# Kernel tuning notes

Hardware: AMD Instinct MI355X
Metric: run time of the kernel (lower is better)

## Reference

```python
import jax, jax.numpy as jnp
import numpy as np


def setup_inputs() -> dict:
    key = jax.random.key(0)
    k1, k2 = jax.random.split(key)
    B, La, Lb, D = 32, 512, 512, 768
    a_bar = jax.random.normal(k1, (B, La, D), dtype=jnp.float32)
    b_bar = jax.random.normal(k2, (B, Lb, D), dtype=jnp.float32)
    return {"a_bar": a_bar, "b_bar": b_bar}


def reference(a_bar, b_bar):
    # e: [B, La, Lb] cross-attention scores
    e = jnp.einsum('bad,bcd->bac', a_bar, b_bar)
    # attend over b positions (softmax dim=2) -> aligned representation of a
    a_tilde = jnp.einsum('bac,bcd->bad', jax.nn.softmax(e, axis=2), b_bar)
    # attend over a positions (softmax dim=1), transpose, bmm with a_bar
    b_tilde = jnp.einsum('bac,bad->bcd', jax.nn.softmax(e, axis=1), a_bar)
    m_a = jnp.concatenate([a_bar, a_tilde, a_bar - a_tilde, a_bar * a_tilde], axis=-1)
    m_b = jnp.concatenate([b_bar, b_tilde, b_bar - b_tilde, b_bar * b_tilde], axis=-1)
    return (m_a, m_b)
```

## Files before the change

kernel.cpp:

```cpp
#include <hip/hip_runtime.h>
#include <hip/hip_bf16.h>
#include <math.h>

#define NB 32
#define LA 512
#define LB 512
#define DD 768

typedef __bf16 bf16x4 __attribute__((ext_vector_type(4)));
typedef __bf16 bf16x8 __attribute__((ext_vector_type(8)));
typedef float f32x4 __attribute__((ext_vector_type(4)));

#define LSTR 40

__global__ __launch_bounds__(256) void gemm_e_mfma(
    const float* __restrict__ A, const float* __restrict__ Bm,
    float* __restrict__ E) {
  __shared__ __bf16 Ah[128][LSTR], Al[128][LSTR];
  __shared__ __bf16 Bh[128][LSTR], Bl[128][LSTR];

  const int b = blockIdx.z;
  const int i0 = blockIdx.x * 128, j0 = blockIdx.y * 128;
  const float* Ab = A + (size_t)b * LA * DD;
  const float* Bb = Bm + (size_t)b * LB * DD;
  float* Eb = E + (size_t)b * LA * LB;

  const int t = threadIdx.x;
  const int lane = t & 63, wave = t >> 6;
  const int wm = (wave >> 1) * 64, wn = (wave & 1) * 64;
  const int quad = lane >> 4, l16 = lane & 15;
  const int sr = t >> 3, sc = t & 7;

  f32x4 acc[4][4] = {};

  for (int k0 = 0; k0 < DD; k0 += 32) {
    float4 av[4], bv[4];
#pragma unroll
    for (int p = 0; p < 4; ++p) {
      av[p] = *(const float4*)(Ab + (size_t)(i0 + sr + p * 32) * DD + k0 + sc * 4);
      bv[p] = *(const float4*)(Bb + (size_t)(j0 + sr + p * 32) * DD + k0 + sc * 4);
    }
    __syncthreads();
#pragma unroll
    for (int p = 0; p < 4; ++p) {
      const int m = sr + p * 32;
      float va[4] = {av[p].x, av[p].y, av[p].z, av[p].w};
      float vb[4] = {bv[p].x, bv[p].y, bv[p].z, bv[p].w};
      bf16x4 ha, la, hb, lb;
#pragma unroll
      for (int q = 0; q < 4; ++q) {
        __bf16 h = (__bf16)va[q];
        ha[q] = h; la[q] = (__bf16)(va[q] - (float)h);
        h = (__bf16)vb[q];
        hb[q] = h; lb[q] = (__bf16)(vb[q] - (float)h);
      }
      *(bf16x4*)&Ah[m][sc * 4] = ha; *(bf16x4*)&Al[m][sc * 4] = la;
      *(bf16x4*)&Bh[m][sc * 4] = hb; *(bf16x4*)&Bl[m][sc * 4] = lb;
    }
    __syncthreads();

    bf16x8 fah[4], fal[4], fbh[4], fbl[4];
#pragma unroll
    for (int f = 0; f < 4; ++f) {
      fah[f] = *(bf16x8*)&Ah[wm + f * 16 + l16][quad * 8];
      fal[f] = *(bf16x8*)&Al[wm + f * 16 + l16][quad * 8];
      fbh[f] = *(bf16x8*)&Bh[wn + f * 16 + l16][quad * 8];
      fbl[f] = *(bf16x8*)&Bl[wn + f * 16 + l16][quad * 8];
    }
#pragma unroll
    for (int fm = 0; fm < 4; ++fm)
#pragma unroll
      for (int fn = 0; fn < 4; ++fn) {
        acc[fm][fn] = __builtin_amdgcn_mfma_f32_16x16x32_bf16(fah[fm], fbh[fn], acc[fm][fn], 0, 0, 0);
        acc[fm][fn] = __builtin_amdgcn_mfma_f32_16x16x32_bf16(fah[fm], fbl[fn], acc[fm][fn], 0, 0, 0);
        acc[fm][fn] = __builtin_amdgcn_mfma_f32_16x16x32_bf16(fal[fm], fbh[fn], acc[fm][fn], 0, 0, 0);
      }
  }

#pragma unroll
  for (int fm = 0; fm < 4; ++fm)
#pragma unroll
    for (int r = 0; r < 4; ++r) {
      const int i = i0 + wm + fm * 16 + quad * 4 + r;
#pragma unroll
      for (int fn = 0; fn < 4; ++fn)
        Eb[(size_t)i * LB + j0 + wn + fn * 16 + l16] = acc[fm][fn][r];
    }
}

__global__ __launch_bounds__(256) void row_stats_kernel(
    const float* __restrict__ E, float* __restrict__ rmax,
    float* __restrict__ rsum) {
  const int wave = threadIdx.x >> 6;
  const int lane = threadIdx.x & 63;
  const int row = blockIdx.x * 4 + wave;
  const float* Er = E + (size_t)row * LB;
  float vals[8];
  float m = -INFINITY;
#pragma unroll
  for (int c = 0; c < 8; ++c) {
    vals[c] = Er[lane + c * 64];
    m = fmaxf(m, vals[c]);
  }
#pragma unroll
  for (int off = 32; off > 0; off >>= 1) m = fmaxf(m, __shfl_xor(m, off));
  float s = 0.f;
#pragma unroll
  for (int c = 0; c < 8; ++c) s += __expf(vals[c] - m);
#pragma unroll
  for (int off = 32; off > 0; off >>= 1) s += __shfl_xor(s, off);
  if (lane == 0) { rmax[row] = m; rsum[row] = s; }
}

__global__ __launch_bounds__(256) void col_stats_kernel(
    const float* __restrict__ E, float* __restrict__ cmax,
    float* __restrict__ csum) {
  const int b = blockIdx.y;
  const int j = blockIdx.x * 256 + threadIdx.x;
  const float* Eb = E + (size_t)b * LA * LB;
  float m = -INFINITY, s = 0.f;
  for (int i = 0; i < LA; ++i) {
    const float v = Eb[(size_t)i * LB + j];
    const float mn = fmaxf(m, v);
    s = s * __expf(m - mn) + __expf(v - mn);
    m = mn;
  }
  cmax[b * LB + j] = m;
  csum[b * LB + j] = s;
}

__global__ __launch_bounds__(256) void gemm_at_mfma(
    const float* __restrict__ E, const float* __restrict__ Bm,
    const float* __restrict__ A, const float* __restrict__ rmax,
    const float* __restrict__ rsum, float* __restrict__ Ma) {
  __shared__ __bf16 Ps[128][LSTR];
  __shared__ __bf16 Bs[128][LSTR];
  __shared__ float rm_s[128], rs_s[128];

  const int b = blockIdx.z;
  const int i0 = blockIdx.x * 128, d0 = blockIdx.y * 128;
  const float* Eb = E + (size_t)b * LA * LB;
  const float* Bb = Bm + (size_t)b * LB * DD;
  const float* Ab = A + (size_t)b * LA * DD;

  const int t = threadIdx.x;
  const int lane = t & 63, wave = t >> 6;
  const int wm = (wave >> 1) * 64, wn = (wave & 1) * 64;
  const int quad = lane >> 4, l16 = lane & 15;
  const int sr = t >> 3, sc = t & 7;
  const int jr = t >> 3, jc = t & 7;

  if (t < 128) {
    rm_s[t] = rmax[b * LA + i0 + t];
    rs_s[t] = 1.f / rsum[b * LA + i0 + t];
  }
  __syncthreads();

  f32x4 acc[4][4] = {};

  for (int k0 = 0; k0 < LB; k0 += 32) {
    float4 ev[4], bv[4];
#pragma unroll
    for (int p = 0; p < 4; ++p) {
      ev[p] = *(const float4*)(Eb + (size_t)(i0 + sr + p * 32) * LB + k0 + sc * 4);
      bv[p] = *(const float4*)(Bb + (size_t)(k0 + jr) * DD + d0 + p * 32 + jc * 4);
    }
    __syncthreads();
#pragma unroll
    for (int p = 0; p < 4; ++p) {
      const int m = sr + p * 32;
      const float rmv = rm_s[m], rsv = rs_s[m];
      float v[4] = {ev[p].x, ev[p].y, ev[p].z, ev[p].w};
      bf16x4 pb;
#pragma unroll
      for (int q = 0; q < 4; ++q) pb[q] = (__bf16)(__expf(v[q] - rmv) * rsv);
      *(bf16x4*)&Ps[m][sc * 4] = pb;
      float w[4] = {bv[p].x, bv[p].y, bv[p].z, bv[p].w};
#pragma unroll
      for (int q = 0; q < 4; ++q) Bs[p * 32 + jc * 4 + q][jr] = (__bf16)w[q];
    }
    __syncthreads();

    bf16x8 fa[4], fb[4];
#pragma unroll
    for (int f = 0; f < 4; ++f) {
      fa[f] = *(bf16x8*)&Ps[wm + f * 16 + l16][quad * 8];
      fb[f] = *(bf16x8*)&Bs[wn + f * 16 + l16][quad * 8];
    }
#pragma unroll
    for (int fm = 0; fm < 4; ++fm)
#pragma unroll
      for (int fn = 0; fn < 4; ++fn)
        acc[fm][fn] = __builtin_amdgcn_mfma_f32_16x16x32_bf16(fa[fm], fb[fn], acc[fm][fn], 0, 0, 0);
  }

#pragma unroll
  for (int fm = 0; fm < 4; ++fm)
#pragma unroll
    for (int r = 0; r < 4; ++r) {
      const int i = i0 + wm + fm * 16 + quad * 4 + r;
      float* base = Ma + ((size_t)b * LA + i) * (4 * DD);
#pragma unroll
      for (int fn = 0; fn < 4; ++fn) {
        const int d = d0 + wn + fn * 16 + l16;
        const float av = Ab[(size_t)i * DD + d];
        const float at = acc[fm][fn][r];
        base[d] = av;
        base[DD + d] = at;
        base[2 * DD + d] = av - at;
        base[3 * DD + d] = av * at;
      }
    }
}

__global__ __launch_bounds__(256) void gemm_bt_mfma(
    const float* __restrict__ E, const float* __restrict__ A,
    const float* __restrict__ Bm, const float* __restrict__ cmax,
    const float* __restrict__ csum, float* __restrict__ Mb) {
  __shared__ __bf16 Ps[128][LSTR];
  __shared__ __bf16 As[128][LSTR];
  __shared__ float cm_s[128], cs_s[128];

  const int b = blockIdx.z;
  const int j0 = blockIdx.x * 128, d0 = blockIdx.y * 128;
  const float* Eb = E + (size_t)b * LA * LB;
  const float* Ab = A + (size_t)b * LA * DD;
  const float* Bb = Bm + (size_t)b * LB * DD;

  const int t = threadIdx.x;
  const int lane = t & 63, wave = t >> 6;
  const int wm = (wave >> 1) * 64, wn = (wave & 1) * 64;
  const int quad = lane >> 4, l16 = lane & 15;
  const int ir = t >> 3, ic = t & 7;

  if (t < 128) {
    cm_s[t] = cmax[b * LB + j0 + t];
    cs_s[t] = 1.f / csum[b * LB + j0 + t];
  }
  __syncthreads();

  f32x4 acc[4][4] = {};

  for (int k0 = 0; k0 < LA; k0 += 32) {
    float4 ev[4], av[4];
#pragma unroll
    for (int p = 0; p < 4; ++p) {
      ev[p] = *(const float4*)(Eb + (size_t)(k0 + ir) * LB + j0 + p * 32 + ic * 4);
      av[p] = *(const float4*)(Ab + (size_t)(k0 + ir) * DD + d0 + p * 32 + ic * 4);
    }
    __syncthreads();
#pragma unroll
    for (int p = 0; p < 4; ++p) {
      const float4 cm4 = *(const float4*)&cm_s[p * 32 + ic * 4];
      const float4 cs4 = *(const float4*)&cs_s[p * 32 + ic * 4];
      float v[4] = {ev[p].x, ev[p].y, ev[p].z, ev[p].w};
      float cmv[4] = {cm4.x, cm4.y, cm4.z, cm4.w};
      float csv[4] = {cs4.x, cs4.y, cs4.z, cs4.w};
      float w[4] = {av[p].x, av[p].y, av[p].z, av[p].w};
#pragma unroll
      for (int q = 0; q < 4; ++q) {
        Ps[p * 32 + ic * 4 + q][ir] = (__bf16)(__expf(v[q] - cmv[q]) * csv[q]);
        As[p * 32 + ic * 4 + q][ir] = (__bf16)w[q];
      }
    }
    __syncthreads();

    bf16x8 fa[4], fb[4];
#pragma unroll
    for (int f = 0; f < 4; ++f) {
      fa[f] = *(bf16x8*)&Ps[wm + f * 16 + l16][quad * 8];
      fb[f] = *(bf16x8*)&As[wn + f * 16 + l16][quad * 8];
    }
#pragma unroll
    for (int fm = 0; fm < 4; ++fm)
#pragma unroll
      for (int fn = 0; fn < 4; ++fn)
        acc[fm][fn] = __builtin_amdgcn_mfma_f32_16x16x32_bf16(fa[fm], fb[fn], acc[fm][fn], 0, 0, 0);
  }

#pragma unroll
  for (int fm = 0; fm < 4; ++fm)
#pragma unroll
    for (int r = 0; r < 4; ++r) {
      const int j = j0 + wm + fm * 16 + quad * 4 + r;
      float* base = Mb + ((size_t)b * LB + j) * (4 * DD);
#pragma unroll
      for (int fn = 0; fn < 4; ++fn) {
        const int d = d0 + wn + fn * 16 + l16;
        const float bvv = Bb[(size_t)j * DD + d];
        const float bt = acc[fm][fn][r];
        base[d] = bvv;
        base[DD + d] = bt;
        base[2 * DD + d] = bvv - bt;
        base[3 * DD + d] = bvv * bt;
      }
    }
}

extern "C" void kernel_launch(void* const* d_in, const int* in_sizes, int n_in,
                              void* d_out, int out_size, void* d_ws,
                              size_t ws_size, hipStream_t stream) {
  const float* a = (const float*)d_in[0];
  const float* bb = (const float*)d_in[1];
  float* out = (float*)d_out;
  float* Ma = out;
  float* Mb = out + (size_t)NB * LA * 4 * DD;

  float* E = (float*)d_ws;
  float* rmax = (float*)((char*)d_ws + (size_t)NB * LA * LB * sizeof(float));
  float* rsum = rmax + NB * LA;
  float* cmax = rsum + NB * LA;
  float* csum = cmax + NB * LB;

  gemm_e_mfma<<<dim3(LA / 128, LB / 128, NB), 256, 0, stream>>>(a, bb, E);
  row_stats_kernel<<<dim3(NB * LA / 4), 256, 0, stream>>>(E, rmax, rsum);
  col_stats_kernel<<<dim3(LB / 256, NB), 256, 0, stream>>>(E, cmax, csum);
  gemm_at_mfma<<<dim3(LA / 128, DD / 128, NB), 256, 0, stream>>>(E, bb, a, rmax,
                                                                 rsum, Ma);
  gemm_bt_mfma<<<dim3(LB / 128, DD / 128, NB), 256, 0, stream>>>(E, a, bb, cmax,
                                                                 csum, Mb);
}
```

Before: 656.3 us.

## Precompute bf16 hi/lo and transposed operands, use direct-to-LDS loads, split column stats

```diff
diff --git a/kernel.cpp b/kernel.cpp
--- a/kernel.cpp
+++ b/kernel.cpp
@@ -13,59 +13,98 @@
 
 #define LSTR 40
 
+__device__ __forceinline__ void gload_lds16(const void* g, void* l) {
+  __builtin_amdgcn_global_load_lds(
+      (const __attribute__((address_space(1))) unsigned int*)g,
+      (__attribute__((address_space(3))) unsigned int*)l, 16, 0, 0);
+}
+
+__global__ __launch_bounds__(256) void convert_kernel(
+    const float* __restrict__ A, const float* __restrict__ B,
+    __bf16* __restrict__ Ah, __bf16* __restrict__ Al,
+    __bf16* __restrict__ Bh, __bf16* __restrict__ Bl,
+    __bf16* __restrict__ AhT, __bf16* __restrict__ BhT) {
+  const int zb = blockIdx.z;
+  const int b = zb & (NB - 1);
+  const bool isB = zb >= NB;
+  const float* src = (isB ? B : A) + (size_t)b * 512 * DD;
+  __bf16* H = (isB ? Bh : Ah) + (size_t)b * 512 * DD;
+  __bf16* L = (isB ? Bl : Al) + (size_t)b * 512 * DD;
+  __bf16* T = (isB ? BhT : AhT) + (size_t)b * DD * 512;
+  const int d0 = blockIdx.x * 64, i0 = blockIdx.y * 64;
+  __shared__ __bf16 Tt[64][72];
+  const int t = threadIdx.x;
+  const int c4 = t & 15, r = t >> 4;
+#pragma unroll
+  for (int p = 0; p < 4; ++p) {
+    const int i = i0 + r + p * 16;
+    const float4 v = *(const float4*)(src + (size_t)i * DD + d0 + c4 * 4);
+    float vv[4] = {v.x, v.y, v.z, v.w};
+    bf16x4 h, l;
+#pragma unroll
+    for (int q = 0; q < 4; ++q) {
+      h[q] = (__bf16)vv[q];
+      l[q] = (__bf16)(vv[q] - (float)h[q]);
+    }
+    *(bf16x4*)(H + (size_t)i * DD + d0 + c4 * 4) = h;
+    *(bf16x4*)(L + (size_t)i * DD + d0 + c4 * 4) = l;
+#pragma unroll
+    for (int q = 0; q < 4; ++q) Tt[c4 * 4 + q][r + p * 16] = h[q];
+  }
+  __syncthreads();
+  const int cc = t & 7, rr = t >> 3;
+#pragma unroll
+  for (int p = 0; p < 2; ++p) {
+    const int d = d0 + rr + p * 32;
+    *(bf16x8*)(T + (size_t)d * 512 + i0 + cc * 8) =
+        *(bf16x8*)&Tt[rr + p * 32][cc * 8];
+  }
+}
+
 __global__ __launch_bounds__(256) void gemm_e_mfma(
-    const float* __restrict__ A, const float* __restrict__ Bm,
+    const __bf16* __restrict__ Ah, const __bf16* __restrict__ Al,
+    const __bf16* __restrict__ Bh, const __bf16* __restrict__ Bl,
     float* __restrict__ E) {
-  __shared__ __bf16 Ah[128][LSTR], Al[128][LSTR];
-  __shared__ __bf16 Bh[128][LSTR], Bl[128][LSTR];
+  __shared__ __bf16 AhS[128][32], AlS[128][32], BhS[128][32], BlS[128][32];
 
   const int b = blockIdx.z;
   const int i0 = blockIdx.x * 128, j0 = blockIdx.y * 128;
-  const float* Ab = A + (size_t)b * LA * DD;
-  const float* Bb = Bm + (size_t)b * LB * DD;
+  const __bf16* AhB = Ah + (size_t)b * LA * DD;
+  const __bf16* AlB = Al + (size_t)b * LA * DD;
+  const __bf16* BhB = Bh + (size_t)b * LB * DD;
+  const __bf16* BlB = Bl + (size_t)b * LB * DD;
   float* Eb = E + (size_t)b * LA * LB;
 
   const int t = threadIdx.x;
   const int lane = t & 63, wave = t >> 6;
   const int wm = (wave >> 1) * 64, wn = (wave & 1) * 64;
   const int quad = lane >> 4, l16 = lane & 15;
-  const int sr = t >> 3, sc = t & 7;
+  const int lrow = lane >> 2, lcol = (lane & 3) * 8;
 
   f32x4 acc[4][4] = {};
 
   for (int k0 = 0; k0 < DD; k0 += 32) {
-    float4 av[4], bv[4];
-#pragma unroll
-    for (int p = 0; p < 4; ++p) {
-      av[p] = *(const float4*)(Ab + (size_t)(i0 + sr + p * 32) * DD + k0 + sc * 4);
-      bv[p] = *(const float4*)(Bb + (size_t)(j0 + sr + p * 32) * DD + k0 + sc * 4);
-    }
-    __syncthreads();
-#pragma unroll
-    for (int p = 0; p < 4; ++p) {
-      const int m = sr + p * 32;
-      float va[4] = {av[p].x, av[p].y, av[p].z, av[p].w};
-      float vb[4] = {bv[p].x, bv[p].y, bv[p].z, bv[p].w};
-      bf16x4 ha, la, hb, lb;
-#pragma unroll
-      for (int q = 0; q < 4; ++q) {
-        __bf16 h = (__bf16)va[q];
-        ha[q] = h; la[q] = (__bf16)(va[q] - (float)h);
-        h = (__bf16)vb[q];
-        hb[q] = h; lb[q] = (__bf16)(vb[q] - (float)h);
-      }
-      *(bf16x4*)&Ah[m][sc * 4] = ha; *(bf16x4*)&Al[m][sc * 4] = la;
-      *(bf16x4*)&Bh[m][sc * 4] = hb; *(bf16x4*)&Bl[m][sc * 4] = lb;
+    __syncthreads();
+#pragma unroll
+    for (int n = 0; n < 2; ++n) {
+      const int c = n * 4 + wave;
+      const int row = c * 16 + lrow;
+      const size_t gA = (size_t)(i0 + row) * DD + k0 + lcol;
+      const size_t gB = (size_t)(j0 + row) * DD + k0 + lcol;
+      gload_lds16(AhB + gA, (char*)&AhS[0][0] + c * 1024);
+      gload_lds16(AlB + gA, (char*)&AlS[0][0] + c * 1024);
+      gload_lds16(BhB + gB, (char*)&BhS[0][0] + c * 1024);
+      gload_lds16(BlB + gB, (char*)&BlS[0][0] + c * 1024);
     }
     __syncthreads();
 
     bf16x8 fah[4], fal[4], fbh[4], fbl[4];
 #pragma unroll
     for (int f = 0; f < 4; ++f) {
-      fah[f] = *(bf16x8*)&Ah[wm + f * 16 + l16][quad * 8];
-      fal[f] = *(bf16x8*)&Al[wm + f * 16 + l16][quad * 8];
-      fbh[f] = *(bf16x8*)&Bh[wn + f * 16 + l16][quad * 8];
-      fbl[f] = *(bf16x8*)&Bl[wn + f * 16 + l16][quad * 8];
+      fah[f] = *(bf16x8*)&AhS[wm + f * 16 + l16][quad * 8];
+      fal[f] = *(bf16x8*)&AlS[wm + f * 16 + l16][quad * 8];
+      fbh[f] = *(bf16x8*)&BhS[wn + f * 16 + l16][quad * 8];
+      fbl[f] = *(bf16x8*)&BlS[wn + f * 16 + l16][quad * 8];
     }
 #pragma unroll
     for (int fm = 0; fm < 4; ++fm)
@@ -112,35 +151,54 @@
   if (lane == 0) { rmax[row] = m; rsum[row] = s; }
 }
 
-__global__ __launch_bounds__(256) void col_stats_kernel(
-    const float* __restrict__ E, float* __restrict__ cmax,
-    float* __restrict__ csum) {
-  const int b = blockIdx.y;
-  const int j = blockIdx.x * 256 + threadIdx.x;
-  const float* Eb = E + (size_t)b * LA * LB;
+__global__ __launch_bounds__(256) void col_partial(
+    const float* __restrict__ E, float* __restrict__ pcm,
+    float* __restrict__ pcs) {
+  const int c = blockIdx.x * 256 + threadIdx.x;
+  const int b = c >> 9, j = c & (LB - 1);
+  const int i0 = blockIdx.y * 64;
+  const float* Ep = E + ((size_t)b * LA + i0) * LB + j;
   float m = -INFINITY, s = 0.f;
-  for (int i = 0; i < LA; ++i) {
-    const float v = Eb[(size_t)i * LB + j];
+#pragma unroll 4
+  for (int i = 0; i < 64; ++i) {
+    const float v = Ep[(size_t)i * LB];
     const float mn = fmaxf(m, v);
     s = s * __expf(m - mn) + __expf(v - mn);
     m = mn;
   }
-  cmax[b * LB + j] = m;
-  csum[b * LB + j] = s;
+  pcm[blockIdx.y * (NB * LB) + c] = m;
+  pcs[blockIdx.y * (NB * LB) + c] = s;
+}
+
+__global__ __launch_bounds__(256) void col_combine(
+    const float* __restrict__ pcm, const float* __restrict__ pcs,
+    float* __restrict__ cmax, float* __restrict__ csum) {
+  const int c = blockIdx.x * 256 + threadIdx.x;
+  float m = -INFINITY, s = 0.f;
+#pragma unroll
+  for (int p = 0; p < 8; ++p) {
+    const float mp = pcm[p * (NB * LB) + c];
+    const float sp = pcs[p * (NB * LB) + c];
+    const float mn = fmaxf(m, mp);
+    s = s * __expf(m - mn) + sp * __expf(mp - mn);
+    m = mn;
+  }
+  cmax[c] = m;
+  csum[c] = s;
 }
 
 __global__ __launch_bounds__(256) void gemm_at_mfma(
-    const float* __restrict__ E, const float* __restrict__ Bm,
+    const float* __restrict__ E, const __bf16* __restrict__ BhT,
     const float* __restrict__ A, const float* __restrict__ rmax,
     const float* __restrict__ rsum, float* __restrict__ Ma) {
   __shared__ __bf16 Ps[128][LSTR];
-  __shared__ __bf16 Bs[128][LSTR];
+  __shared__ __bf16 Bs[128][32];
   __shared__ float rm_s[128], rs_s[128];
 
   const int b = blockIdx.z;
   const int i0 = blockIdx.x * 128, d0 = blockIdx.y * 128;
   const float* Eb = E + (size_t)b * LA * LB;
-  const float* Bb = Bm + (size_t)b * LB * DD;
+  const __bf16* Tb = BhT + (size_t)b * DD * LB;
   const float* Ab = A + (size_t)b * LA * DD;
 
   const int t = threadIdx.x;
@@ -148,7 +206,7 @@
   const int wm = (wave >> 1) * 64, wn = (wave & 1) * 64;
   const int quad = lane >> 4, l16 = lane & 15;
   const int sr = t >> 3, sc = t & 7;
-  const int jr = t >> 3, jc = t & 7;
+  const int lrow = lane >> 2, lcol = (lane & 3) * 8;
 
   if (t < 128) {
     rm_s[t] = rmax[b * LA + i0 + t];
@@ -159,13 +217,17 @@
   f32x4 acc[4][4] = {};
 
   for (int k0 = 0; k0 < LB; k0 += 32) {
-    float4 ev[4], bv[4];
-#pragma unroll
-    for (int p = 0; p < 4; ++p) {
+    float4 ev[4];
+#pragma unroll
+    for (int p = 0; p < 4; ++p)
       ev[p] = *(const float4*)(Eb + (size_t)(i0 + sr + p * 32) * LB + k0 + sc * 4);
-      bv[p] = *(const float4*)(Bb + (size_t)(k0 + jr) * DD + d0 + p * 32 + jc * 4);
-    }
-    __syncthreads();
+    __syncthreads();
+#pragma unroll
+    for (int n = 0; n < 2; ++n) {
+      const int c = n * 4 + wave;
+      gload_lds16(Tb + (size_t)(d0 + c * 16 + lrow) * LB + k0 + lcol,
+                  (char*)&Bs[0][0] + c * 1024);
+    }
 #pragma unroll
     for (int p = 0; p < 4; ++p) {
       const int m = sr + p * 32;
@@ -175,9 +237,6 @@
 #pragma unroll
       for (int q = 0; q < 4; ++q) pb[q] = (__bf16)(__expf(v[q] - rmv) * rsv);
       *(bf16x4*)&Ps[m][sc * 4] = pb;
-      float w[4] = {bv[p].x, bv[p].y, bv[p].z, bv[p].w};
-#pragma unroll
-      for (int q = 0; q < 4; ++q) Bs[p * 32 + jc * 4 + q][jr] = (__bf16)w[q];
     }
     __syncthreads();
 
@@ -214,17 +273,17 @@
 }
 
 __global__ __launch_bounds__(256) void gemm_bt_mfma(
-    const float* __restrict__ E, const float* __restrict__ A,
+    const float* __restrict__ E, const __bf16* __restrict__ AhT,
     const float* __restrict__ Bm, const float* __restrict__ cmax,
     const float* __restrict__ csum, float* __restrict__ Mb) {
   __shared__ __bf16 Ps[128][LSTR];
-  __shared__ __bf16 As[128][LSTR];
+  __shared__ __bf16 As[128][32];
   __shared__ float cm_s[128], cs_s[128];
 
   const int b = blockIdx.z;
   const int j0 = blockIdx.x * 128, d0 = blockIdx.y * 128;
   const float* Eb = E + (size_t)b * LA * LB;
-  const float* Ab = A + (size_t)b * LA * DD;
+  const __bf16* Tb = AhT + (size_t)b * DD * LA;
   const float* Bb = Bm + (size_t)b * LB * DD;
 
   const int t = threadIdx.x;
@@ -232,6 +291,7 @@
   const int wm = (wave >> 1) * 64, wn = (wave & 1) * 64;
   const int quad = lane >> 4, l16 = lane & 15;
   const int ir = t >> 3, ic = t & 7;
+  const int lrow = lane >> 2, lcol = (lane & 3) * 8;
 
   if (t < 128) {
     cm_s[t] = cmax[b * LB + j0 + t];
@@ -242,13 +302,17 @@
   f32x4 acc[4][4] = {};
 
   for (int k0 = 0; k0 < LA; k0 += 32) {
-    float4 ev[4], av[4];
-#pragma unroll
-    for (int p = 0; p < 4; ++p) {
+    float4 ev[4];
+#pragma unroll
+    for (int p = 0; p < 4; ++p)
       ev[p] = *(const float4*)(Eb + (size_t)(k0 + ir) * LB + j0 + p * 32 + ic * 4);
-      av[p] = *(const float4*)(Ab + (size_t)(k0 + ir) * DD + d0 + p * 32 + ic * 4);
-    }
-    __syncthreads();
+    __syncthreads();
+#pragma unroll
+    for (int n = 0; n < 2; ++n) {
+      const int c = n * 4 + wave;
+      gload_lds16(Tb + (size_t)(d0 + c * 16 + lrow) * LA + k0 + lcol,
+                  (char*)&As[0][0] + c * 1024);
+    }
 #pragma unroll
     for (int p = 0; p < 4; ++p) {
       const float4 cm4 = *(const float4*)&cm_s[p * 32 + ic * 4];
@@ -256,12 +320,9 @@
       float v[4] = {ev[p].x, ev[p].y, ev[p].z, ev[p].w};
       float cmv[4] = {cm4.x, cm4.y, cm4.z, cm4.w};
       float csv[4] = {cs4.x, cs4.y, cs4.z, cs4.w};
-      float w[4] = {av[p].x, av[p].y, av[p].z, av[p].w};
-#pragma unroll
-      for (int q = 0; q < 4; ++q) {
+#pragma unroll
+      for (int q = 0; q < 4; ++q)
         Ps[p * 32 + ic * 4 + q][ir] = (__bf16)(__expf(v[q] - cmv[q]) * csv[q]);
-        As[p * 32 + ic * 4 + q][ir] = (__bf16)w[q];
-      }
     }
     __syncthreads();
 
@@ -306,17 +367,29 @@
   float* Ma = out;
   float* Mb = out + (size_t)NB * LA * 4 * DD;
 
-  float* E = (float*)d_ws;
-  float* rmax = (float*)((char*)d_ws + (size_t)NB * LA * LB * sizeof(float));
-  float* rsum = rmax + NB * LA;
-  float* cmax = rsum + NB * LA;
-  float* csum = cmax + NB * LB;
-
-  gemm_e_mfma<<<dim3(LA / 128, LB / 128, NB), 256, 0, stream>>>(a, bb, E);
+  char* p = (char*)d_ws;
+  float* E = (float*)p;      p += (size_t)NB * LA * LB * 4;
+  float* rmax = (float*)p;   p += (size_t)NB * LA * 4;
+  float* rsum = (float*)p;   p += (size_t)NB * LA * 4;
+  float* cmax = (float*)p;   p += (size_t)NB * LB * 4;
+  float* csum = (float*)p;   p += (size_t)NB * LB * 4;
+  float* pcm = (float*)p;    p += (size_t)8 * NB * LB * 4;
+  float* pcs = (float*)p;    p += (size_t)8 * NB * LB * 4;
+  __bf16* Ah = (__bf16*)p;   p += (size_t)NB * LA * DD * 2;
+  __bf16* Al = (__bf16*)p;   p += (size_t)NB * LA * DD * 2;
+  __bf16* Bh = (__bf16*)p;   p += (size_t)NB * LB * DD * 2;
+  __bf16* Bl = (__bf16*)p;   p += (size_t)NB * LB * DD * 2;
+  __bf16* AhT = (__bf16*)p;  p += (size_t)NB * DD * LA * 2;
+  __bf16* BhT = (__bf16*)p;  p += (size_t)NB * DD * LB * 2;
+
+  convert_kernel<<<dim3(DD / 64, 512 / 64, 2 * NB), 256, 0, stream>>>(
+      a, bb, Ah, Al, Bh, Bl, AhT, BhT);
+  gemm_e_mfma<<<dim3(LA / 128, LB / 128, NB), 256, 0, stream>>>(Ah, Al, Bh, Bl, E);
   row_stats_kernel<<<dim3(NB * LA / 4), 256, 0, stream>>>(E, rmax, rsum);
-  col_stats_kernel<<<dim3(LB / 256, NB), 256, 0, stream>>>(E, cmax, csum);
-  gemm_at_mfma<<<dim3(LA / 128, DD / 128, NB), 256, 0, stream>>>(E, bb, a, rmax,
+  col_partial<<<dim3(NB * LB / 256, 8), 256, 0, stream>>>(E, pcm, pcs);
+  col_combine<<<dim3(NB * LB / 256), 256, 0, stream>>>(pcm, pcs, cmax, csum);
+  gemm_at_mfma<<<dim3(LA / 128, DD / 128, NB), 256, 0, stream>>>(E, BhT, a, rmax,
                                                                  rsum, Ma);
-  gemm_bt_mfma<<<dim3(LB / 128, DD / 128, NB), 256, 0, stream>>>(E, a, bb, cmax,
+  gemm_bt_mfma<<<dim3(LB / 128, DD / 128, NB), 256, 0, stream>>>(E, AhT, bb, cmax,
                                                                  csum, Mb);
 }
```

After: 685.3 us. +4.4%, slower.
